# Kernel optimization log

Hardware: AMD Instinct MI355X
Metric: run time of the kernel (lower is better)

Reference implementation:

```python
import jax, jax.numpy as jnp
import numpy as np


def setup_inputs() -> dict:
    key = jax.random.key(0)
    k1, k2, k3, k4 = jax.random.split(key, 4)
    B, H, S, D = 2, 16, 2048, 64
    q = jax.random.normal(k1, (B, H, S, D), dtype=jnp.float32)
    k = jax.random.normal(k2, (B, H, S, D), dtype=jnp.float32)
    v = jax.random.normal(k3, (B, H, S, D), dtype=jnp.float32)
    mask = jax.random.randint(k4, (1, 1, S, S), 0, 2, dtype=jnp.int32)
    return {"q": q, "k": k, "v": v, "mask": mask}


def reference(q, k, v, mask):
    # scores: [B,H,S,S] -- intentionally materialized as in the original
    d = k.shape[-1]
    scale = 1.0 / jnp.sqrt(jnp.asarray(d, dtype=q.dtype))
    x = jnp.einsum("bhqd,bhkd->bhqk", q, k) * scale
    x = x + mask.astype(x.dtype) * jnp.asarray(-10000.0, dtype=x.dtype)
    p = jax.nn.softmax(x, axis=-1)  # dropout is identity in eval mode
    return jnp.einsum("bhqk,bhkd->bhqd", p, v)
```

## Files before the change

kernel.cpp:

```cpp
#include <hip/hip_runtime.h>


#define S_LEN 2048
#define D_DIM 64
#define N_KT 32
#define NBH 32
#define FRAG_SHORTS 4096

typedef __attribute__((ext_vector_type(8))) short bf16x8;
typedef __attribute__((ext_vector_type(16))) float f32x16;
typedef __attribute__((ext_vector_type(2))) __fp16 fp16x2;
typedef unsigned int u32;
typedef unsigned long long u64;

#define C1 0.180336880111121f
#define CM (-14426.9504088896f)

static __device__ __forceinline__ unsigned short f2bf(float f) {
  union { float f; unsigned u; } x; x.f = f;
  return (unsigned short)((x.u + 0x8000u) >> 16);
}
static __device__ __forceinline__ unsigned packbf(float lo, float hi) {
  union { float f; unsigned u; } a, b; a.f = lo; b.f = hi;
  return ((a.u + 0x8000u) >> 16) | ((b.u + 0x8000u) & 0xffff0000u);
}
static __device__ __forceinline__ f32x16 zero16() {
  f32x16 z;
#pragma unroll
  for (int i = 0; i < 16; ++i) z[i] = 0.f;
  return z;
}
static __device__ __forceinline__ unsigned pkh(float lo, float hi) {
  union { fp16x2 h; unsigned u; } x;
  x.h = __builtin_amdgcn_cvt_pkrtz(lo, hi);
  return x.u;
}

__global__ __launch_bounds__(256) void prep_kv(
    const float* __restrict__ k, const float* __restrict__ v,
    unsigned short* __restrict__ kws, unsigned short* __restrict__ vws) {
  const int kt = blockIdx.x, bh = blockIdx.y;
  const int t = threadIdx.x;
  __shared__ unsigned short Kr[64 * 72];
  __shared__ unsigned short Vr[64 * 72];
  const size_t goff = (size_t)bh * (S_LEN * D_DIM) + (size_t)kt * 64 * D_DIM;
  const float4* kg = (const float4*)(k + goff);
  const float4* vg = (const float4*)(v + goff);
#pragma unroll
  for (int j = 0; j < 4; ++j) {
    const int i = t + j * 256;
    const int row = i >> 4, c4 = i & 15;
    const float4 x = kg[i];
    ushort4 w;
    w.x = f2bf(x.x); w.y = f2bf(x.y); w.z = f2bf(x.z); w.w = f2bf(x.w);
    *(ushort4*)&Kr[row * 72 + c4 * 4] = w;
    const float4 y = vg[i];
    const unsigned p01 = pkh(y.x, y.y), p23 = pkh(y.z, y.w);
    uint2 vv; vv.x = p01; vv.y = p23;
    *(uint2*)&Vr[row * 72 + c4 * 4] = vv;
  }
  __syncthreads();
  uint4* kimg4 = (uint4*)(kws + (size_t)(bh * N_KT + kt) * FRAG_SHORTS);
  for (int c = t; c < 512; c += 256) {
    const int col = c & 31, hlc = (c >> 5) & 1, ks = (c >> 6) & 3, khc = c >> 8;
    kimg4[c] = *(const uint4*)&Kr[(khc * 32 + col) * 72 + ks * 16 + hlc * 8];
  }
  uint4* vimg4 = (uint4*)(vws + (size_t)(bh * N_KT + kt) * FRAG_SHORTS);
  for (int c = t; c < 512; c += 256) {
    const int col = c & 31, b = (c >> 5) & 1, hlc = (c >> 6) & 1, kcHi = c >> 7;
    const int d = b * 32 + col, kk = (2 * kcHi + hlc) * 8;
    union { unsigned short s[8]; uint4 u; } o;
#pragma unroll
    for (int jj = 0; jj < 8; ++jj) o.s[jj] = Vr[(kk + jj) * 72 + d];
    vimg4[c] = o.u;
  }
}

__global__ __launch_bounds__(256) void prep_mask(
    const int* __restrict__ mask, u32* __restrict__ mw) {
  const int gt = blockIdx.x * 256 + threadIdx.x;
  const int row = gt >> 9;
  const int qi = gt & 511;
  const int4 m = *(const int4*)(mask + (size_t)row * S_LEN + qi * 4);
  const int kt = qi >> 4;
  const int j = (qi << 2) & 63;
  const int kb = j >> 5, g = (j >> 3) & 3, hl = (j >> 2) & 1;
  u32 w0 = 0, w1 = 0;
  if (m.x == 0) w0 |= 0x0000FFFFu;
  if (m.y == 0) w0 |= 0xFFFF0000u;
  if (m.z == 0) w1 |= 0x0000FFFFu;
  if (m.w == 0) w1 |= 0xFFFF0000u;
  uint2 wv; wv.x = w0; wv.y = w1;
  *(uint2*)&mw[((size_t)(row * 2 + hl) * N_KT + kt) * 16 + kb * 8 + g * 2] = wv;
}

__global__ __launch_bounds__(256, 3) void attn_fwd(
    const float* __restrict__ q, const unsigned short* __restrict__ kws,
    const unsigned short* __restrict__ vws, const u32* __restrict__ mw,
    float* __restrict__ out) {
  const int qt = blockIdx.x;
  const int bh = blockIdx.y;
  const size_t hoff = (size_t)bh * (S_LEN * D_DIM);

  const int t = threadIdx.x;
  const int wave = t >> 6;
  const int lane = t & 63;
  const int col = lane & 31;
  const int hl = lane >> 5;
  const int qh = wave >> 1;
  const int kh = wave & 1;

  const int qg = qt * 64 + qh * 32 + col;

  bf16x8 bQ[4];
  {
    const float* qrow = q + hoff + (size_t)qg * D_DIM;
#pragma unroll
    for (int ks = 0; ks < 4; ++ks) {
      const float4 x0 = *(const float4*)(qrow + ks * 16 + hl * 8);
      const float4 x1 = *(const float4*)(qrow + ks * 16 + hl * 8 + 4);
      union { bf16x8 v; unsigned d[4]; } u;
      u.d[0] = packbf(x0.x * C1, x0.y * C1);
      u.d[1] = packbf(x0.z * C1, x0.w * C1);
      u.d[2] = packbf(x1.x * C1, x1.y * C1);
      u.d[3] = packbf(x1.z * C1, x1.w * C1);
      bQ[ks] = u.v;
    }
  }

  f32x16 oT0 = zero16(), oT1 = zero16();
  float lacc = 0.f;
  const uint4* mrow = (const uint4*)(mw + (size_t)(qg * 2 + hl) * N_KT * 16);

  const unsigned short* kL =
      kws + (size_t)bh * N_KT * FRAG_SHORTS + kh * 2048 + hl * 256 + col * 8;
  const unsigned short* vL =
      vws + (size_t)bh * N_KT * FRAG_SHORTS + kh * 2048 + hl * 512 + col * 8;

#define LDK8(kt_, ks_) (*(const bf16x8*)(kL + (size_t)(kt_) * FRAG_SHORTS + (ks_) * 512))
#define LDV8(kt_, ks2_, b_) \
  (*(const bf16x8*)(vL + (size_t)(kt_) * FRAG_SHORTS + (ks2_) * 1024 + (b_) * 256))

#if __has_builtin(__builtin_amdgcn_fdot2)
  const fp16x2 ones2 = {(__fp16)1.0f, (__fp16)1.0f};
#endif

  auto body = [&](bf16x8 k0, bf16x8 k1, bf16x8 k2, bf16x8 k3, int kt) {
    const bf16x8 v00 = LDV8(kt, 0, 0), v01 = LDV8(kt, 0, 1);
    const bf16x8 v10 = LDV8(kt, 1, 0), v11 = LDV8(kt, 1, 1);
    const uint4 mq0 = mrow[kt * 4 + kh * 2 + 0];
    const uint4 mq1 = mrow[kt * 4 + kh * 2 + 1];

    f32x16 sT = zero16();
    sT = __builtin_amdgcn_mfma_f32_32x32x16_bf16(k0, bQ[0], sT, 0, 0, 0);
    sT = __builtin_amdgcn_mfma_f32_32x32x16_bf16(k1, bQ[1], sT, 0, 0, 0);
    sT = __builtin_amdgcn_mfma_f32_32x32x16_bf16(k2, bQ[2], sT, 0, 0, 0);
    sT = __builtin_amdgcn_mfma_f32_32x32x16_bf16(k3, bQ[3], sT, 0, 0, 0);

    const u32 mwv[8] = {mq0.x, mq0.y, mq0.z, mq0.w,
                        mq1.x, mq1.y, mq1.z, mq1.w};
    unsigned pw[8];
#pragma unroll
    for (int g2 = 0; g2 < 4; ++g2) {
      const float e0 = __builtin_amdgcn_exp2f(sT[g2 * 4 + 0]);
      const float e1 = __builtin_amdgcn_exp2f(sT[g2 * 4 + 1]);
      const float e2 = __builtin_amdgcn_exp2f(sT[g2 * 4 + 2]);
      const float e3 = __builtin_amdgcn_exp2f(sT[g2 * 4 + 3]);
#if __has_builtin(__builtin_amdgcn_fdot2)
      const unsigned w0 = pkh(e0, e1) & mwv[g2 * 2 + 0];
      const unsigned w1 = pkh(e2, e3) & mwv[g2 * 2 + 1];
      pw[g2 * 2 + 0] = w0;
      pw[g2 * 2 + 1] = w1;
      union { unsigned u; fp16x2 h; } c0, c1;
      c0.u = w0; c1.u = w1;
      lacc = __builtin_amdgcn_fdot2(c0.h, ones2, lacc, false);
      lacc = __builtin_amdgcn_fdot2(c1.h, ones2, lacc, false);
#else
      const u32 mlo = mwv[g2 * 2 + 0], mhi = mwv[g2 * 2 + 1];
      const float e0m = (mlo & 0xFFFFu) ? e0 : 0.f;
      const float e1m = (mlo >> 16) ? e1 : 0.f;
      const float e2m = (mhi & 0xFFFFu) ? e2 : 0.f;
      const float e3m = (mhi >> 16) ? e3 : 0.f;
      pw[g2 * 2 + 0] = pkh(e0m, e1m);
      pw[g2 * 2 + 1] = pkh(e2m, e3m);
      lacc += (e0m + e1m) + (e2m + e3m);
#endif
    }

#pragma unroll
    for (int ks2 = 0; ks2 < 2; ++ks2) {
      const unsigned d0 = pw[4 * ks2 + 0], d1 = pw[4 * ks2 + 1];
      const unsigned d2 = pw[4 * ks2 + 2], d3 = pw[4 * ks2 + 3];
      const unsigned s0 = hl ? d0 : d2;
      const unsigned s1 = hl ? d1 : d3;
      const unsigned r0 = (unsigned)__shfl_xor((int)s0, 32);
      const unsigned r1 = (unsigned)__shfl_xor((int)s1, 32);
      union { bf16x8 v; unsigned d[4]; } pf;
      pf.d[0] = hl ? r0 : d0;
      pf.d[1] = hl ? r1 : d1;
      pf.d[2] = hl ? d2 : r0;
      pf.d[3] = hl ? d3 : r1;
      const bf16x8 aV0 = ks2 ? v10 : v00;
      const bf16x8 aV1 = ks2 ? v11 : v01;
      oT0 = __builtin_amdgcn_mfma_f32_32x32x16_f16(aV0, pf.v, oT0, 0, 0, 0);
      oT1 = __builtin_amdgcn_mfma_f32_32x32x16_f16(aV1, pf.v, oT1, 0, 0, 0);
    }
  };

  bf16x8 ka0 = LDK8(0, 0), ka1 = LDK8(0, 1), ka2 = LDK8(0, 2), ka3 = LDK8(0, 3);
  bf16x8 kb0, kb1, kb2, kb3;
  for (int kt = 0; kt < N_KT; kt += 2) {
    kb0 = LDK8(kt + 1, 0); kb1 = LDK8(kt + 1, 1);
    kb2 = LDK8(kt + 1, 2); kb3 = LDK8(kt + 1, 3);
    body(ka0, ka1, ka2, ka3, kt);
    if (kt + 2 < N_KT) {
      ka0 = LDK8(kt + 2, 0); ka1 = LDK8(kt + 2, 1);
      ka2 = LDK8(kt + 2, 2); ka3 = LDK8(kt + 2, 3);
    }
    body(kb0, kb1, kb2, kb3, kt + 1);
  }
#undef LDK8
#undef LDV8

  __shared__ float xb[64 * 68];
  __shared__ float lb[64];
  const float l2 = lacc + __shfl_xor(lacc, 32);
  float* xr = xb + (size_t)(qh * 32 + col) * 68;
  if (kh) {
#pragma unroll
    for (int rg = 0; rg < 4; ++rg) {
      float4 w0, w1;
      w0.x = oT0[rg * 4 + 0]; w0.y = oT0[rg * 4 + 1];
      w0.z = oT0[rg * 4 + 2]; w0.w = oT0[rg * 4 + 3];
      w1.x = oT1[rg * 4 + 0]; w1.y = oT1[rg * 4 + 1];
      w1.z = oT1[rg * 4 + 2]; w1.w = oT1[rg * 4 + 3];
      *(float4*)(xr + 8 * rg + 4 * hl) = w0;
      *(float4*)(xr + 32 + 8 * rg + 4 * hl) = w1;
    }
    if (!hl) lb[qh * 32 + col] = l2;
  }
  __syncthreads();
  if (!kh) {
    const float inv = 1.0f / (l2 + lb[qh * 32 + col]);
    float* orow = out + hoff + (size_t)qg * D_DIM;
#pragma unroll
    for (int rg = 0; rg < 4; ++rg) {
      const float4 a0 = *(const float4*)(xr + 8 * rg + 4 * hl);
      const float4 a1 = *(const float4*)(xr + 32 + 8 * rg + 4 * hl);
      float4 w0, w1;
      w0.x = (oT0[rg * 4 + 0] + a0.x) * inv;
      w0.y = (oT0[rg * 4 + 1] + a0.y) * inv;
      w0.z = (oT0[rg * 4 + 2] + a0.z) * inv;
      w0.w = (oT0[rg * 4 + 3] + a0.w) * inv;
      w1.x = (oT1[rg * 4 + 0] + a1.x) * inv;
      w1.y = (oT1[rg * 4 + 1] + a1.y) * inv;
      w1.z = (oT1[rg * 4 + 2] + a1.z) * inv;
      w1.w = (oT1[rg * 4 + 3] + a1.w) * inv;
      *(float4*)(orow + 8 * rg + 4 * hl) = w0;
      *(float4*)(orow + 32 + 8 * rg + 4 * hl) = w1;
    }
  }
}

#define LDK 72
#define LDV 72
__global__ __launch_bounds__(256, 2) void attn_fwd_self(
    const float* __restrict__ q, const float* __restrict__ k,
    const float* __restrict__ v, const int* __restrict__ mask,
    float* __restrict__ out) {
  const int qt = blockIdx.x;
  const int bh = blockIdx.y;
  const size_t hoff = (size_t)bh * (S_LEN * D_DIM);
  __shared__ unsigned short Ks[64 * LDK];
  __shared__ unsigned short Vt[64 * LDV];
  const int t = threadIdx.x;
  const int wave = t >> 6;
  const int lane = t & 63;
  const int col = lane & 31;
  const int hl = lane >> 5;
  const int sw = col >> 2;
  const int qg = qt * 128 + wave * 32 + col;
  bf16x8 bQ[4];
  {
    const float* qrow = q + hoff + (size_t)qg * D_DIM;
#pragma unroll
    for (int ks = 0; ks < 4; ++ks) {
      const float4 x0 = *(const float4*)(qrow + ks * 16 + hl * 8);
      const float4 x1 = *(const float4*)(qrow + ks * 16 + hl * 8 + 4);
      union { bf16x8 v; unsigned d[4]; } u;
      u.d[0] = packbf(x0.x, x0.y);
      u.d[1] = packbf(x0.z, x0.w);
      u.d[2] = packbf(x1.x, x1.y);
      u.d[3] = packbf(x1.z, x1.w);
      bQ[ks] = u.v;
    }
  }
  float4 pk[4], pv[4];
  {
    const float4* kg = (const float4*)(k + hoff);
    const float4* vg = (const float4*)(v + hoff);
#pragma unroll
    for (int j = 0; j < 4; ++j) { pk[j] = kg[t + j * 256]; pv[j] = vg[t + j * 256]; }
  }
  f32x16 oT0 = zero16(), oT1 = zero16();
  float lacc = 0.f;
  const int* mrow = mask + (size_t)qg * S_LEN;
  for (int kt = 0; kt < N_KT; ++kt) {
    __syncthreads();
#pragma unroll
    for (int j = 0; j < 4; ++j) {
      const int i = t + j * 256;
      const int row = i >> 4, c4 = i & 15;
      ushort4 w;
      w.x = f2bf(pk[j].x); w.y = f2bf(pk[j].y);
      w.z = f2bf(pk[j].z); w.w = f2bf(pk[j].w);
      *(ushort4*)&Ks[row * LDK + c4 * 4] = w;
      const int swc = 8 * (((row >> 3) + c4) & 7) + (row & 7);
      Vt[(4 * c4 + 0) * LDV + swc] = f2bf(pv[j].x);
      Vt[(4 * c4 + 1) * LDV + swc] = f2bf(pv[j].y);
      Vt[(4 * c4 + 2) * LDV + swc] = f2bf(pv[j].z);
      Vt[(4 * c4 + 3) * LDV + swc] = f2bf(pv[j].w);
    }
    __syncthreads();
    if (kt + 1 < N_KT) {
      const float4* kg = (const float4*)(k + hoff + (size_t)(kt + 1) * 64 * D_DIM);
      const float4* vg = (const float4*)(v + hoff + (size_t)(kt + 1) * 64 * D_DIM);
#pragma unroll
      for (int j = 0; j < 4; ++j) { pk[j] = kg[t + j * 256]; pv[j] = vg[t + j * 256]; }
    }
    int4 mq[2][4];
#pragma unroll
    for (int kb = 0; kb < 2; ++kb)
#pragma unroll
      for (int g = 0; g < 4; ++g)
        mq[kb][g] = *(const int4*)(mrow + kt * 64 + kb * 32 + g * 8 + hl * 4);
    f32x16 sT0 = zero16(), sT1 = zero16();
#pragma unroll
    for (int ks = 0; ks < 4; ++ks) {
      const bf16x8 aK0 = *(const bf16x8*)&Ks[col * LDK + ks * 16 + hl * 8];
      const bf16x8 aK1 = *(const bf16x8*)&Ks[(32 + col) * LDK + ks * 16 + hl * 8];
      sT0 = __builtin_amdgcn_mfma_f32_32x32x16_bf16(aK0, bQ[ks], sT0, 0, 0, 0);
      sT1 = __builtin_amdgcn_mfma_f32_32x32x16_bf16(aK1, bQ[ks], sT1, 0, 0, 0);
    }
    unsigned pw[2][8];
#pragma unroll
    for (int kb = 0; kb < 2; ++kb) {
      const f32x16 sT = kb ? sT1 : sT0;
      float e[16];
#pragma unroll
      for (int g = 0; g < 4; ++g) {
        const int4 mv = mq[kb][g];
        const int* mvp = &mv.x;
#pragma unroll
        for (int r3 = 0; r3 < 4; ++r3) {
          const int reg = g * 4 + r3;
          const float bias = mvp[r3] ? CM : 0.0f;
          const float ev = __builtin_amdgcn_exp2f(fmaf(sT[reg], C1, bias));
          e[reg] = ev;
          lacc += ev;
        }
        pw[kb][g * 2 + 0] = packbf(e[g * 4 + 0], e[g * 4 + 1]);
        pw[kb][g * 2 + 1] = packbf(e[g * 4 + 2], e[g * 4 + 3]);
      }
    }
#pragma unroll
    for (int ks = 0; ks < 4; ++ks) {
      const int kb = ks >> 1, h = ks & 1;
      const unsigned d0 = pw[kb][4 * h + 0], d1 = pw[kb][4 * h + 1];
      const unsigned d2 = pw[kb][4 * h + 2], d3 = pw[kb][4 * h + 3];
      const unsigned s0 = hl ? d0 : d2;
      const unsigned s1 = hl ? d1 : d3;
      const unsigned r0 = (unsigned)__shfl_xor((int)s0, 32);
      const unsigned r1 = (unsigned)__shfl_xor((int)s1, 32);
      union { bf16x8 v; unsigned d[4]; } pf;
      pf.d[0] = hl ? r0 : d0;
      pf.d[1] = hl ? r1 : d1;
      pf.d[2] = hl ? d2 : r0;
      pf.d[3] = hl ? d3 : r1;
      const int cpr = 8 * (((2 * ks + hl) + sw) & 7);
      const bf16x8 aV0 = *(const bf16x8*)&Vt[col * LDV + cpr];
      const bf16x8 aV1 = *(const bf16x8*)&Vt[(32 + col) * LDV + cpr];
      oT0 = __builtin_amdgcn_mfma_f32_32x32x16_bf16(aV0, pf.v, oT0, 0, 0, 0);
      oT1 = __builtin_amdgcn_mfma_f32_32x32x16_bf16(aV1, pf.v, oT1, 0, 0, 0);
    }
  }
  const float ltot = lacc + __shfl_xor(lacc, 32);
  const float inv = 1.0f / ltot;
  float* orow = out + hoff + (size_t)qg * D_DIM;
#pragma unroll
  for (int rg = 0; rg < 4; ++rg) {
    float4 w0, w1;
    w0.x = oT0[rg * 4 + 0] * inv; w0.y = oT0[rg * 4 + 1] * inv;
    w0.z = oT0[rg * 4 + 2] * inv; w0.w = oT0[rg * 4 + 3] * inv;
    w1.x = oT1[rg * 4 + 0] * inv; w1.y = oT1[rg * 4 + 1] * inv;
    w1.z = oT1[rg * 4 + 2] * inv; w1.w = oT1[rg * 4 + 3] * inv;
    *(float4*)(orow + 8 * rg + 4 * hl) = w0;
    *(float4*)(orow + 32 + 8 * rg + 4 * hl) = w1;
  }
}

extern "C" void kernel_launch(void* const* d_in, const int* in_sizes, int n_in,
                              void* d_out, int out_size, void* d_ws, size_t ws_size,
                              hipStream_t stream) {
  const float* q = (const float*)d_in[0];
  const float* k = (const float*)d_in[1];
  const float* v = (const float*)d_in[2];
  const int* mask = (const int*)d_in[3];
  float* out = (float*)d_out;

  const size_t img_shorts = (size_t)NBH * N_KT * FRAG_SHORTS;
  const size_t mw_words = (size_t)S_LEN * 2 * N_KT * 16;
  const size_t need = img_shorts * 2 * sizeof(unsigned short) + mw_words * 4;

  if (ws_size >= need) {
    unsigned short* kws = (unsigned short*)d_ws;
    unsigned short* vws = kws + img_shorts;
    u32* mwp = (u32*)(vws + img_shorts);
    prep_kv<<<dim3(N_KT, NBH), dim3(256), 0, stream>>>(k, v, kws, vws);
    prep_mask<<<dim3((S_LEN * (S_LEN / 4)) / 256), dim3(256), 0, stream>>>(mask, mwp);
    attn_fwd<<<dim3(S_LEN / 64, NBH), dim3(256), 0, stream>>>(q, kws, vws, mwp, out);
  } else {
    attn_fwd_self<<<dim3(S_LEN / 128, NBH), dim3(256), 0, stream>>>(q, k, v, mask, out);
  }
}
```

Measured before the change: 179.9 us.

## Stage interleaved K/V tiles through double-buffered LDS in attention kernel

K and V fragment images are interleaved into one contiguous tile per key block. The attention kernel now loads each tile cooperatively into a double-buffered shared memory region, prefetching two tiles ahead in registers, instead of every wave reading its fragments directly from global memory. The mask-prep kernel is rewritten so each thread writes a full 16-byte word, and the row-sum accumulator is split in two to shorten the dependency chain. This aims to cut redundant global/L2 traffic, since all four waves of a block previously fetched the same K/V fragments, at the cost of 32KB of LDS, a block barrier per key tile, and possible occupancy loss.

```diff
diff --git a/kernel.cpp b/kernel.cpp
--- a/kernel.cpp
+++ b/kernel.cpp
@@ -5,7 +5,7 @@
 #define D_DIM 64
 #define N_KT 32
 #define NBH 32
-#define FRAG_SHORTS 4096
+#define TILE_KV_SHORTS 8192
 
 typedef __attribute__((ext_vector_type(8))) short bf16x8;
 typedef __attribute__((ext_vector_type(16))) float f32x16;
@@ -38,7 +38,7 @@
 
 __global__ __launch_bounds__(256) void prep_kv(
     const float* __restrict__ k, const float* __restrict__ v,
-    unsigned short* __restrict__ kws, unsigned short* __restrict__ vws) {
+    unsigned short* __restrict__ kvws) {
   const int kt = blockIdx.x, bh = blockIdx.y;
   const int t = threadIdx.x;
   __shared__ unsigned short Kr[64 * 72];
@@ -60,47 +60,50 @@
     *(uint2*)&Vr[row * 72 + c4 * 4] = vv;
   }
   __syncthreads();
-  uint4* kimg4 = (uint4*)(kws + (size_t)(bh * N_KT + kt) * FRAG_SHORTS);
+  uint4* img = (uint4*)(kvws + (size_t)(bh * N_KT + kt) * TILE_KV_SHORTS);
   for (int c = t; c < 512; c += 256) {
     const int col = c & 31, hlc = (c >> 5) & 1, ks = (c >> 6) & 3, khc = c >> 8;
-    kimg4[c] = *(const uint4*)&Kr[(khc * 32 + col) * 72 + ks * 16 + hlc * 8];
-  }
-  uint4* vimg4 = (uint4*)(vws + (size_t)(bh * N_KT + kt) * FRAG_SHORTS);
+    img[c] = *(const uint4*)&Kr[(khc * 32 + col) * 72 + ks * 16 + hlc * 8];
+  }
   for (int c = t; c < 512; c += 256) {
     const int col = c & 31, b = (c >> 5) & 1, hlc = (c >> 6) & 1, kcHi = c >> 7;
     const int d = b * 32 + col, kk = (2 * kcHi + hlc) * 8;
     union { unsigned short s[8]; uint4 u; } o;
 #pragma unroll
     for (int jj = 0; jj < 8; ++jj) o.s[jj] = Vr[(kk + jj) * 72 + d];
-    vimg4[c] = o.u;
+    img[512 + c] = o.u;
   }
 }
 
 __global__ __launch_bounds__(256) void prep_mask(
     const int* __restrict__ mask, u32* __restrict__ mw) {
   const int gt = blockIdx.x * 256 + threadIdx.x;
-  const int row = gt >> 9;
-  const int qi = gt & 511;
-  const int4 m = *(const int4*)(mask + (size_t)row * S_LEN + qi * 4);
-  const int kt = qi >> 4;
-  const int j = (qi << 2) & 63;
-  const int kb = j >> 5, g = (j >> 3) & 3, hl = (j >> 2) & 1;
-  u32 w0 = 0, w1 = 0;
-  if (m.x == 0) w0 |= 0x0000FFFFu;
-  if (m.y == 0) w0 |= 0xFFFF0000u;
-  if (m.z == 0) w1 |= 0x0000FFFFu;
-  if (m.w == 0) w1 |= 0xFFFF0000u;
-  uint2 wv; wv.x = w0; wv.y = w1;
-  *(uint2*)&mw[((size_t)(row * 2 + hl) * N_KT + kt) * 16 + kb * 8 + g * 2] = wv;
+  const int q4 = gt & 3;
+  const int kt = (gt >> 2) & 31;
+  const int hl = (gt >> 7) & 1;
+  const int row = gt >> 8;
+  const int j0 = kt * 64 + 32 * (q4 >> 1) + 16 * (q4 & 1) + 4 * hl;
+  const int* mr = mask + (size_t)row * S_LEN;
+  const int4 a = *(const int4*)(mr + j0);
+  const int4 b = *(const int4*)(mr + j0 + 8);
+  uint4 w;
+  w.x = (a.x == 0 ? 0x0000FFFFu : 0u) | (a.y == 0 ? 0xFFFF0000u : 0u);
+  w.y = (a.z == 0 ? 0x0000FFFFu : 0u) | (a.w == 0 ? 0xFFFF0000u : 0u);
+  w.z = (b.x == 0 ? 0x0000FFFFu : 0u) | (b.y == 0 ? 0xFFFF0000u : 0u);
+  w.w = (b.z == 0 ? 0x0000FFFFu : 0u) | (b.w == 0 ? 0xFFFF0000u : 0u);
+  *(uint4*)&mw[((size_t)(row * 2 + hl) * N_KT + kt) * 16 + q4 * 4] = w;
 }
 
 __global__ __launch_bounds__(256, 3) void attn_fwd(
-    const float* __restrict__ q, const unsigned short* __restrict__ kws,
-    const unsigned short* __restrict__ vws, const u32* __restrict__ mw,
-    float* __restrict__ out) {
+    const float* __restrict__ q, const unsigned short* __restrict__ kvws,
+    const u32* __restrict__ mw, float* __restrict__ out) {
   const int qt = blockIdx.x;
   const int bh = blockIdx.y;
   const size_t hoff = (size_t)bh * (S_LEN * D_DIM);
+
+  __shared__ unsigned short sbuf[2][TILE_KV_SHORTS];
+  __shared__ float xb[64 * 68];
+  __shared__ float lb[64];
 
   const int t = threadIdx.x;
   const int wave = t >> 6;
@@ -129,33 +132,52 @@
   }
 
   f32x16 oT0 = zero16(), oT1 = zero16();
-  float lacc = 0.f;
+  float lacc0 = 0.f, lacc1 = 0.f;
   const uint4* mrow = (const uint4*)(mw + (size_t)(qg * 2 + hl) * N_KT * 16);
-
-  const unsigned short* kL =
-      kws + (size_t)bh * N_KT * FRAG_SHORTS + kh * 2048 + hl * 256 + col * 8;
-  const unsigned short* vL =
-      vws + (size_t)bh * N_KT * FRAG_SHORTS + kh * 2048 + hl * 512 + col * 8;
-
-#define LDK8(kt_, ks_) (*(const bf16x8*)(kL + (size_t)(kt_) * FRAG_SHORTS + (ks_) * 512))
-#define LDV8(kt_, ks2_, b_) \
-  (*(const bf16x8*)(vL + (size_t)(kt_) * FRAG_SHORTS + (ks2_) * 1024 + (b_) * 256))
+  const uint4* kvt = (const uint4*)(kvws + (size_t)bh * N_KT * TILE_KV_SHORTS);
 
 #if __has_builtin(__builtin_amdgcn_fdot2)
   const fp16x2 ones2 = {(__fp16)1.0f, (__fp16)1.0f};
 #endif
 
-  auto body = [&](bf16x8 k0, bf16x8 k1, bf16x8 k2, bf16x8 k3, int kt) {
-    const bf16x8 v00 = LDV8(kt, 0, 0), v01 = LDV8(kt, 0, 1);
-    const bf16x8 v10 = LDV8(kt, 1, 0), v11 = LDV8(kt, 1, 1);
+  uint4 st[4];
+#pragma unroll
+  for (int i = 0; i < 4; ++i) st[i] = kvt[t + i * 256];
+  {
+    uint4* lw = (uint4*)&sbuf[0][0];
+#pragma unroll
+    for (int i = 0; i < 4; ++i) lw[t + i * 256] = st[i];
+  }
+#pragma unroll
+  for (int i = 0; i < 4; ++i) st[i] = kvt[1024 + t + i * 256];
+  __syncthreads();
+
+  for (int kt = 0; kt < N_KT; ++kt) {
+    const int p = kt & 1;
+    if (kt + 1 < N_KT) {
+      uint4* lw = (uint4*)&sbuf[p ^ 1][0];
+#pragma unroll
+      for (int i = 0; i < 4; ++i) lw[t + i * 256] = st[i];
+    }
+    if (kt + 2 < N_KT) {
+      const uint4* gg = kvt + (size_t)(kt + 2) * 1024;
+#pragma unroll
+      for (int i = 0; i < 4; ++i) st[i] = gg[t + i * 256];
+    }
+
     const uint4 mq0 = mrow[kt * 4 + kh * 2 + 0];
     const uint4 mq1 = mrow[kt * 4 + kh * 2 + 1];
 
+    const unsigned short* Kb = &sbuf[p][0];
+    const unsigned short* Vb = &sbuf[p][4096];
+
     f32x16 sT = zero16();
-    sT = __builtin_amdgcn_mfma_f32_32x32x16_bf16(k0, bQ[0], sT, 0, 0, 0);
-    sT = __builtin_amdgcn_mfma_f32_32x32x16_bf16(k1, bQ[1], sT, 0, 0, 0);
-    sT = __builtin_amdgcn_mfma_f32_32x32x16_bf16(k2, bQ[2], sT, 0, 0, 0);
-    sT = __builtin_amdgcn_mfma_f32_32x32x16_bf16(k3, bQ[3], sT, 0, 0, 0);
+#pragma unroll
+    for (int ks = 0; ks < 4; ++ks) {
+      const bf16x8 aK =
+          *(const bf16x8*)&Kb[kh * 2048 + ks * 512 + hl * 256 + col * 8];
+      sT = __builtin_amdgcn_mfma_f32_32x32x16_bf16(aK, bQ[ks], sT, 0, 0, 0);
+    }
 
     const u32 mwv[8] = {mq0.x, mq0.y, mq0.z, mq0.w,
                         mq1.x, mq1.y, mq1.z, mq1.w};
@@ -173,8 +195,8 @@
       pw[g2 * 2 + 1] = w1;
       union { unsigned u; fp16x2 h; } c0, c1;
       c0.u = w0; c1.u = w1;
-      lacc = __builtin_amdgcn_fdot2(c0.h, ones2, lacc, false);
-      lacc = __builtin_amdgcn_fdot2(c1.h, ones2, lacc, false);
+      lacc0 = __builtin_amdgcn_fdot2(c0.h, ones2, lacc0, false);
+      lacc1 = __builtin_amdgcn_fdot2(c1.h, ones2, lacc1, false);
 #else
       const u32 mlo = mwv[g2 * 2 + 0], mhi = mwv[g2 * 2 + 1];
       const float e0m = (mlo & 0xFFFFu) ? e0 : 0.f;
@@ -183,7 +205,8 @@
       const float e3m = (mhi >> 16) ? e3 : 0.f;
       pw[g2 * 2 + 0] = pkh(e0m, e1m);
       pw[g2 * 2 + 1] = pkh(e2m, e3m);
-      lacc += (e0m + e1m) + (e2m + e3m);
+      lacc0 += e0m + e1m;
+      lacc1 += e2m + e3m;
 #endif
     }
 
@@ -200,64 +223,55 @@
       pf.d[1] = hl ? r1 : d1;
       pf.d[2] = hl ? d2 : r0;
       pf.d[3] = hl ? d3 : r1;
-      const bf16x8 aV0 = ks2 ? v10 : v00;
-      const bf16x8 aV1 = ks2 ? v11 : v01;
+      const int kcHi = kh * 2 + ks2;
+      const bf16x8 aV0 =
+          *(const bf16x8*)&Vb[kcHi * 1024 + hl * 512 + 0 * 256 + col * 8];
+      const bf16x8 aV1 =
+          *(const bf16x8*)&Vb[kcHi * 1024 + hl * 512 + 1 * 256 + col * 8];
       oT0 = __builtin_amdgcn_mfma_f32_32x32x16_f16(aV0, pf.v, oT0, 0, 0, 0);
       oT1 = __builtin_amdgcn_mfma_f32_32x32x16_f16(aV1, pf.v, oT1, 0, 0, 0);
     }
-  };
-
-  bf16x8 ka0 = LDK8(0, 0), ka1 = LDK8(0, 1), ka2 = LDK8(0, 2), ka3 = LDK8(0, 3);
-  bf16x8 kb0, kb1, kb2, kb3;
-  for (int kt = 0; kt < N_KT; kt += 2) {
-    kb0 = LDK8(kt + 1, 0); kb1 = LDK8(kt + 1, 1);
-    kb2 = LDK8(kt + 1, 2); kb3 = LDK8(kt + 1, 3);
-    body(ka0, ka1, ka2, ka3, kt);
-    if (kt + 2 < N_KT) {
-      ka0 = LDK8(kt + 2, 0); ka1 = LDK8(kt + 2, 1);
-      ka2 = LDK8(kt + 2, 2); ka3 = LDK8(kt + 2, 3);
-    }
-    body(kb0, kb1, kb2, kb3, kt + 1);
-  }
-#undef LDK8
-#undef LDV8
-
-  __shared__ float xb[64 * 68];
-  __shared__ float lb[64];
-  const float l2 = lacc + __shfl_xor(lacc, 32);
-  float* xr = xb + (size_t)(qh * 32 + col) * 68;
-  if (kh) {
-#pragma unroll
-    for (int rg = 0; rg < 4; ++rg) {
-      float4 w0, w1;
-      w0.x = oT0[rg * 4 + 0]; w0.y = oT0[rg * 4 + 1];
-      w0.z = oT0[rg * 4 + 2]; w0.w = oT0[rg * 4 + 3];
-      w1.x = oT1[rg * 4 + 0]; w1.y = oT1[rg * 4 + 1];
-      w1.z = oT1[rg * 4 + 2]; w1.w = oT1[rg * 4 + 3];
-      *(float4*)(xr + 8 * rg + 4 * hl) = w0;
-      *(float4*)(xr + 32 + 8 * rg + 4 * hl) = w1;
-    }
-    if (!hl) lb[qh * 32 + col] = l2;
-  }
-  __syncthreads();
-  if (!kh) {
-    const float inv = 1.0f / (l2 + lb[qh * 32 + col]);
-    float* orow = out + hoff + (size_t)qg * D_DIM;
-#pragma unroll
-    for (int rg = 0; rg < 4; ++rg) {
-      const float4 a0 = *(const float4*)(xr + 8 * rg + 4 * hl);
-      const float4 a1 = *(const float4*)(xr + 32 + 8 * rg + 4 * hl);
-      float4 w0, w1;
-      w0.x = (oT0[rg * 4 + 0] + a0.x) * inv;
-      w0.y = (oT0[rg * 4 + 1] + a0.y) * inv;
-      w0.z = (oT0[rg * 4 + 2] + a0.z) * inv;
-      w0.w = (oT0[rg * 4 + 3] + a0.w) * inv;
-      w1.x = (oT1[rg * 4 + 0] + a1.x) * inv;
-      w1.y = (oT1[rg * 4 + 1] + a1.y) * inv;
-      w1.z = (oT1[rg * 4 + 2] + a1.z) * inv;
-      w1.w = (oT1[rg * 4 + 3] + a1.w) * inv;
-      *(float4*)(orow + 8 * rg + 4 * hl) = w0;
-      *(float4*)(orow + 32 + 8 * rg + 4 * hl) = w1;
+
+    __syncthreads();
+  }
+
+  {
+    const float lsum = lacc0 + lacc1;
+    const float l2 = lsum + __shfl_xor(lsum, 32);
+    float* xr = xb + (size_t)(qh * 32 + col) * 68;
+    if (kh) {
+#pragma unroll
+      for (int rg = 0; rg < 4; ++rg) {
+        float4 w0, w1;
+        w0.x = oT0[rg * 4 + 0]; w0.y = oT0[rg * 4 + 1];
+        w0.z = oT0[rg * 4 + 2]; w0.w = oT0[rg * 4 + 3];
+        w1.x = oT1[rg * 4 + 0]; w1.y = oT1[rg * 4 + 1];
+        w1.z = oT1[rg * 4 + 2]; w1.w = oT1[rg * 4 + 3];
+        *(float4*)(xr + 8 * rg + 4 * hl) = w0;
+        *(float4*)(xr + 32 + 8 * rg + 4 * hl) = w1;
+      }
+      if (!hl) lb[qh * 32 + col] = l2;
+    }
+    __syncthreads();
+    if (!kh) {
+      const float inv = 1.0f / (l2 + lb[qh * 32 + col]);
+      float* orow = out + hoff + (size_t)qg * D_DIM;
+#pragma unroll
+      for (int rg = 0; rg < 4; ++rg) {
+        const float4 a0 = *(const float4*)(xr + 8 * rg + 4 * hl);
+        const float4 a1 = *(const float4*)(xr + 32 + 8 * rg + 4 * hl);
+        float4 w0, w1;
+        w0.x = (oT0[rg * 4 + 0] + a0.x) * inv;
+        w0.y = (oT0[rg * 4 + 1] + a0.y) * inv;
+        w0.z = (oT0[rg * 4 + 2] + a0.z) * inv;
+        w0.w = (oT0[rg * 4 + 3] + a0.w) * inv;
+        w1.x = (oT1[rg * 4 + 0] + a1.x) * inv;
+        w1.y = (oT1[rg * 4 + 1] + a1.y) * inv;
+        w1.z = (oT1[rg * 4 + 2] + a1.z) * inv;
+        w1.w = (oT1[rg * 4 + 3] + a1.w) * inv;
+        *(float4*)(orow + 8 * rg + 4 * hl) = w0;
+        *(float4*)(orow + 32 + 8 * rg + 4 * hl) = w1;
+      }
     }
   }
 }
@@ -408,17 +422,16 @@
   const int* mask = (const int*)d_in[3];
   float* out = (float*)d_out;
 
-  const size_t img_shorts = (size_t)NBH * N_KT * FRAG_SHORTS;
+  const size_t kv_shorts = (size_t)NBH * N_KT * TILE_KV_SHORTS;
   const size_t mw_words = (size_t)S_LEN * 2 * N_KT * 16;
-  const size_t need = img_shorts * 2 * sizeof(unsigned short) + mw_words * 4;
+  const size_t need = kv_shorts * sizeof(unsigned short) + mw_words * 4;
 
   if (ws_size >= need) {
-    unsigned short* kws = (unsigned short*)d_ws;
-    unsigned short* vws = kws + img_shorts;
-    u32* mwp = (u32*)(vws + img_shorts);
-    prep_kv<<<dim3(N_KT, NBH), dim3(256), 0, stream>>>(k, v, kws, vws);
-    prep_mask<<<dim3((S_LEN * (S_LEN / 4)) / 256), dim3(256), 0, stream>>>(mask, mwp);
-    attn_fwd<<<dim3(S_LEN / 64, NBH), dim3(256), 0, stream>>>(q, kws, vws, mwp, out);
+    unsigned short* kvws = (unsigned short*)d_ws;
+    u32* mwp = (u32*)(kvws + kv_shorts);
+    prep_kv<<<dim3(N_KT, NBH), dim3(256), 0, stream>>>(k, v, kvws);
+    prep_mask<<<dim3((S_LEN * 2 * N_KT * 4) / 256), dim3(256), 0, stream>>>(mask, mwp);
+    attn_fwd<<<dim3(S_LEN / 64, NBH), dim3(256), 0, stream>>>(q, kvws, mwp, out);
   } else {
     attn_fwd_self<<<dim3(S_LEN / 128, NBH), dim3(256), 0, stream>>>(q, k, v, mask, out);
   }
```

Measured after the change: 263.6 us. 1.47x slower.
